# Kernel tuning notes

Measured on AMD Instinct MI355X. Metric: run time of the kernel, lower is better.

## Reference

```python
import jax, jax.numpy as jnp
import numpy as np

B, T, D, H = 2, 2048, 1024, 16
HD = D // H  # head_dim = 64


def setup_inputs() -> dict:
    key = jax.random.key(0)
    k1, k2, k3 = jax.random.split(key, 3)
    s = 0.02
    return {
        "x": jax.random.normal(k1, (B, T, D), dtype=jnp.float32),
        "Wqkv": jax.random.normal(k2, (D, 3 * D), dtype=jnp.float32) * s,
        "bqkv": jnp.zeros((3 * D,), dtype=jnp.float32),
        "Wout": jax.random.normal(k3, (D, D), dtype=jnp.float32) * s,
        "bout": jnp.zeros((D,), dtype=jnp.float32),
    }


def reference(x, Wqkv, bqkv, Wout, bout):
    Bx, Tx, Dx = x.shape
    qkv = x @ Wqkv + bqkv                                  # [B,T,3D]
    qkv = qkv.reshape(Bx, Tx, 3, H, HD)
    q, k, v = (jnp.moveaxis(qkv, 2, 0)[i] for i in range(3))  # each [B,T,H,HD]
    q = q.transpose(0, 2, 1, 3)  # [B,H,T,HD]
    k = k.transpose(0, 2, 1, 3)
    v = v.transpose(0, 2, 1, 3)
    scale = 1.0 / jnp.sqrt(jnp.float32(HD))
    attn = jnp.einsum("bhqd,bhkd->bhqk", q, k) * scale     # [B,H,T,T]
    causal = jnp.tril(jnp.ones((Tx, Tx), dtype=bool))
    attn = jnp.where(causal, attn, -jnp.inf)
    attn = jax.nn.softmax(attn, axis=-1)
    out = jnp.einsum("bhqk,bhkd->bhqd", attn, v)           # [B,H,T,HD]
    out = out.transpose(0, 2, 1, 3).reshape(Bx, Tx, Dx)
    return out @ Wout + bout
```

## Files before the change

### kernel.cpp

```cpp
#include <hip/hip_runtime.h>
#include <hip/hip_bf16.h>

typedef __attribute__((ext_vector_type(8))) short bf16x8;
typedef __attribute__((ext_vector_type(4))) float f32x4;
typedef unsigned short u16;
typedef unsigned int uint;

#define Bb 2
#define Tt 2048
#define Dd 1024
#define Hh 16

__device__ inline u16 f2bf(float f) {
    union { float f; uint u; } v; v.f = f;
    uint r = v.u + 0x7fffu + ((v.u >> 16) & 1u);
    return (u16)(r >> 16);
}

__global__ __launch_bounds__(256) void cvt_bf16(
    const float* __restrict__ in, u16* __restrict__ out)
{
    const size_t i = ((size_t)blockIdx.x * 256 + threadIdx.x) * 8;
    const float4 a = *(const float4*)&in[i];
    const float4 b = *(const float4*)&in[i + 4];
    uint4 o;
    o.x = (uint)f2bf(a.x) | ((uint)f2bf(a.y) << 16);
    o.y = (uint)f2bf(a.z) | ((uint)f2bf(a.w) << 16);
    o.z = (uint)f2bf(b.x) | ((uint)f2bf(b.y) << 16);
    o.w = (uint)f2bf(b.z) | ((uint)f2bf(b.w) << 16);
    *(uint4*)&out[i] = o;
}

__global__ __launch_bounds__(256) void transpose_cvt(
    const float* __restrict__ W, u16* __restrict__ Wt, int K, int N)
{
    __shared__ float tile[64][65];
    const int k0 = blockIdx.y * 64, n0 = blockIdx.x * 64;
    const int tid = threadIdx.x;
    const int tr = tid >> 4;
    const int tc = (tid & 15) * 4;

    #pragma unroll
    for (int i = 0; i < 4; ++i) {
        const float4 v = *(const float4*)&W[(size_t)(k0 + tr + i * 16) * N + n0 + tc];
        tile[tr + i * 16][tc + 0] = v.x;
        tile[tr + i * 16][tc + 1] = v.y;
        tile[tr + i * 16][tc + 2] = v.z;
        tile[tr + i * 16][tc + 3] = v.w;
    }
    __syncthreads();
    #pragma unroll
    for (int i = 0; i < 4; ++i) {
        ushort4 o;
        o.x = f2bf(tile[tc + 0][tr + i * 16]);
        o.y = f2bf(tile[tc + 1][tr + i * 16]);
        o.z = f2bf(tile[tc + 2][tr + i * 16]);
        o.w = f2bf(tile[tc + 3][tr + i * 16]);
        *(ushort4*)&Wt[(size_t)(n0 + tr + i * 16) * K + k0 + tc] = o;
    }
}

__global__ __launch_bounds__(256) void vtrans(
    const u16* __restrict__ qkvb, u16* __restrict__ vglob)
{
    __shared__ u16 ts[64 * 72];
    const int tt = blockIdx.x;
    const int hb = blockIdx.y;
    const int h = hb & 15, b = hb >> 4;
    const int tid = threadIdx.x;
    const int t0 = tt * 64;
    const size_t vbase = (size_t)((b * Hh + h) * 64) * Tt;

    #pragma unroll
    for (int j = 0; j < 2; ++j) {
        const int ci = tid + j * 256;
        const int t = ci >> 3, dc = ci & 7;
        *(int4*)&ts[t * 72 + dc * 8] =
            *(const int4*)&qkvb[(size_t)(b * Tt + t0 + t) * 3072 + 2048 + h * 64 + dc * 8];
    }
    __syncthreads();
    #pragma unroll
    for (int j = 0; j < 2; ++j) {
        const int ci = tid + j * 256;
        const int d = ci >> 3, tc = ci & 7;
        ushort4 lo, hi;
        lo.x = ts[(tc * 8 + 0) * 72 + d];
        lo.y = ts[(tc * 8 + 1) * 72 + d];
        lo.z = ts[(tc * 8 + 2) * 72 + d];
        lo.w = ts[(tc * 8 + 3) * 72 + d];
        hi.x = ts[(tc * 8 + 4) * 72 + d];
        hi.y = ts[(tc * 8 + 5) * 72 + d];
        hi.z = ts[(tc * 8 + 6) * 72 + d];
        hi.w = ts[(tc * 8 + 7) * 72 + d];
        *(ushort4*)&vglob[vbase + (size_t)d * Tt + t0 + tc * 8] = lo;
        *(ushort4*)&vglob[vbase + (size_t)d * Tt + t0 + tc * 8 + 4] = hi;
    }
}

template <int OUT_BF16>
__global__ __launch_bounds__(256) void gemm_bt(
    const u16* __restrict__ A, const u16* __restrict__ Bt,
    const float* __restrict__ bias, void* __restrict__ C,
    int M, int N, int K)
{
    __shared__ u16 As[128 * 40];
    __shared__ u16 Bs[128 * 40];

    const int tid  = threadIdx.x;
    const int lane = tid & 63;
    const int w    = tid >> 6;
    const int wm   = w >> 1, wn = w & 1;
    const int quad = lane >> 4;
    const int m16  = lane & 15;
    const int row0 = blockIdx.y * 128;
    const int col0 = blockIdx.x * 128;

    f32x4 acc[4][4];
    #pragma unroll
    for (int i = 0; i < 4; ++i)
        #pragma unroll
        for (int j = 0; j < 4; ++j) acc[i][j] = (f32x4){0.f, 0.f, 0.f, 0.f};

    const int r0s = tid >> 2,         k0s = tid & 3;
    const int r1s = (tid + 256) >> 2, k1s = tid & 3;

    for (int ko = 0; ko < K; ko += 32) {
        const int4 va0 = *(const int4*)&A [(size_t)(row0 + r0s) * K + ko + k0s * 8];
        const int4 va1 = *(const int4*)&A [(size_t)(row0 + r1s) * K + ko + k1s * 8];
        const int4 vb0 = *(const int4*)&Bt[(size_t)(col0 + r0s) * K + ko + k0s * 8];
        const int4 vb1 = *(const int4*)&Bt[(size_t)(col0 + r1s) * K + ko + k1s * 8];
        __syncthreads();
        *(int4*)&As[r0s * 40 + k0s * 8] = va0;
        *(int4*)&As[r1s * 40 + k1s * 8] = va1;
        *(int4*)&Bs[r0s * 40 + k0s * 8] = vb0;
        *(int4*)&Bs[r1s * 40 + k1s * 8] = vb1;
        __syncthreads();

        bf16x8 af[4], bfr[4];
        #pragma unroll
        for (int mt = 0; mt < 4; ++mt)
            af[mt] = *(const bf16x8*)&As[(wm * 64 + mt * 16 + m16) * 40 + quad * 8];
        #pragma unroll
        for (int nt = 0; nt < 4; ++nt)
            bfr[nt] = *(const bf16x8*)&Bs[(wn * 64 + nt * 16 + m16) * 40 + quad * 8];
        #pragma unroll
        for (int mt = 0; mt < 4; ++mt)
            #pragma unroll
            for (int nt = 0; nt < 4; ++nt)
                acc[mt][nt] = __builtin_amdgcn_mfma_f32_16x16x32_bf16(
                    af[mt], bfr[nt], acc[mt][nt], 0, 0, 0);
    }

    #pragma unroll
    for (int mt = 0; mt < 4; ++mt) {
        #pragma unroll
        for (int nt = 0; nt < 4; ++nt) {
            const int row = row0 + wm * 64 + mt * 16 + quad * 4;
            const int col = col0 + wn * 64 + nt * 16 + m16;
            const float bv = bias[col];
            #pragma unroll
            for (int r = 0; r < 4; ++r) {
                const float v = acc[mt][nt][r] + bv;
                if (OUT_BF16)
                    ((u16*)C)[(size_t)(row + r) * N + col] = f2bf(v);
                else
                    ((float*)C)[(size_t)(row + r) * N + col] = v;
            }
        }
    }
}

__global__ __launch_bounds__(256) void attn_mfma(
    const u16* __restrict__ qkvb, const u16* __restrict__ vglob,
    u16* __restrict__ attn_out)
{
    const int hb  = blockIdx.x;
    const int h   = hb & 15, b = hb >> 4;
    const int qt  = 15 - blockIdx.y;
    const int tid = threadIdx.x;
    const int lane = tid & 63, w = tid >> 6;
    const int quad = lane >> 4, m16 = lane & 15;

    __shared__ u16 S[20480];
    u16* Ks = S;
    u16* Vt = S + 4608;
    u16* Pt = S + 10240;
    u16* Ob = S;

    const int q0 = qt * 128;
    const size_t qkbase = (size_t)(b * Tt) * 3072;
    const size_t vbase  = (size_t)((b * Hh + h) * 64) * Tt;

    bf16x8 qb[2][2];
    #pragma unroll
    for (int nt = 0; nt < 2; ++nt)
        #pragma unroll
        for (int ks = 0; ks < 2; ++ks)
            qb[nt][ks] = *(const bf16x8*)&qkvb[
                qkbase + (size_t)(q0 + w * 32 + nt * 16 + m16) * 3072
                + h * 64 + ks * 32 + quad * 8];

    f32x4 o[4][2];
    #pragma unroll
    for (int ct = 0; ct < 4; ++ct)
        #pragma unroll
        for (int nt = 0; nt < 2; ++nt) o[ct][nt] = (f32x4){0.f, 0.f, 0.f, 0.f};
    float mst[2] = {-__builtin_inff(), -__builtin_inff()};
    float lst[2] = {0.f, 0.f};
    const float scale = 0.125f;

    const int ntiles = 2 * qt + 2;
    for (int kt = 0; kt < ntiles; ++kt) {
        const int k0 = kt * 64;
        __syncthreads();
        #pragma unroll
        for (int j = 0; j < 2; ++j) {
            const int ci = tid + j * 256;
            const int row = ci >> 3, kc = ci & 7;
            *(int4*)&Ks[row * 72 + kc * 8] = *(const int4*)&qkvb[
                qkbase + (size_t)(k0 + row) * 3072 + 1024 + h * 64 + kc * 8];
            *(int4*)&Vt[row * 72 + kc * 8] = *(const int4*)&vglob[
                vbase + (size_t)row * Tt + k0 + kc * 8];
        }
        __syncthreads();

        if (k0 <= q0 + w * 32 + 31) {
            bf16x8 ak[4][2];
            #pragma unroll
            for (int mt = 0; mt < 4; ++mt)
                #pragma unroll
                for (int ks = 0; ks < 2; ++ks)
                    ak[mt][ks] = *(const bf16x8*)&Ks[(mt * 16 + m16) * 72 + ks * 32 + quad * 8];
            f32x4 s[4][2];
            #pragma unroll
            for (int mt = 0; mt < 4; ++mt)
                #pragma unroll
                for (int nt = 0; nt < 2; ++nt) {
                    f32x4 a = (f32x4){0.f, 0.f, 0.f, 0.f};
                    a = __builtin_amdgcn_mfma_f32_16x16x32_bf16(ak[mt][0], qb[nt][0], a, 0, 0, 0);
                    a = __builtin_amdgcn_mfma_f32_16x16x32_bf16(ak[mt][1], qb[nt][1], a, 0, 0, 0);
                    s[mt][nt] = a;
                }

            const int qi0 = q0 + w * 32 + m16;
            if (k0 + 63 > q0 + w * 32) {
                #pragma unroll
                for (int mt = 0; mt < 4; ++mt)
                    #pragma unroll
                    for (int nt = 0; nt < 2; ++nt)
                        #pragma unroll
                        for (int r = 0; r < 4; ++r) {
                            const int key = k0 + mt * 16 + quad * 4 + r;
                            const float v = s[mt][nt][r] * scale;
                            s[mt][nt][r] = (key <= qi0 + nt * 16) ? v : -__builtin_inff();
                        }
            } else {
                #pragma unroll
                for (int mt = 0; mt < 4; ++mt)
                    #pragma unroll
                    for (int nt = 0; nt < 2; ++nt)
                        #pragma unroll
                        for (int r = 0; r < 4; ++r)
                            s[mt][nt][r] *= scale;
            }

            float mx[2] = {-__builtin_inff(), -__builtin_inff()};
            #pragma unroll
            for (int mt = 0; mt < 4; ++mt)
                #pragma unroll
                for (int nt = 0; nt < 2; ++nt)
                    #pragma unroll
                    for (int r = 0; r < 4; ++r)
                        mx[nt] = fmaxf(mx[nt], s[mt][nt][r]);
            #pragma unroll
            for (int nt = 0; nt < 2; ++nt) {
                mx[nt] = fmaxf(mx[nt], __shfl_xor(mx[nt], 16));
                mx[nt] = fmaxf(mx[nt], __shfl_xor(mx[nt], 32));
            }
            float al[2], ls[2];
            #pragma unroll
            for (int nt = 0; nt < 2; ++nt) {
                const float mn = fmaxf(mst[nt], mx[nt]);
                al[nt] = __expf(mst[nt] - mn);
                mst[nt] = mn;
                ls[nt] = 0.f;
            }
            #pragma unroll
            for (int mt = 0; mt < 4; ++mt)
                #pragma unroll
                for (int nt = 0; nt < 2; ++nt) {
                    ushort4 pk;
                    float p0 = __expf(s[mt][nt][0] - mst[nt]);
                    float p1 = __expf(s[mt][nt][1] - mst[nt]);
                    float p2 = __expf(s[mt][nt][2] - mst[nt]);
                    float p3 = __expf(s[mt][nt][3] - mst[nt]);
                    ls[nt] += (p0 + p1) + (p2 + p3);
                    pk.x = f2bf(p0); pk.y = f2bf(p1); pk.z = f2bf(p2); pk.w = f2bf(p3);
                    *(ushort4*)&Pt[(w * 32 + nt * 16 + m16) * 80 + mt * 16 + quad * 4] = pk;
                }
            #pragma unroll
            for (int nt = 0; nt < 2; ++nt) {
                ls[nt] += __shfl_xor(ls[nt], 16);
                ls[nt] += __shfl_xor(ls[nt], 32);
                lst[nt] = lst[nt] * al[nt] + ls[nt];
            }
            #pragma unroll
            for (int ct = 0; ct < 4; ++ct)
                #pragma unroll
                for (int nt = 0; nt < 2; ++nt)
                    #pragma unroll
                    for (int r = 0; r < 4; ++r)
                        o[ct][nt][r] *= al[nt];

            bf16x8 av[4][2], pb[2][2];
            #pragma unroll
            for (int ct = 0; ct < 4; ++ct)
                #pragma unroll
                for (int ks = 0; ks < 2; ++ks)
                    av[ct][ks] = *(const bf16x8*)&Vt[(ct * 16 + m16) * 72 + ks * 32 + quad * 8];
            #pragma unroll
            for (int nt = 0; nt < 2; ++nt)
                #pragma unroll
                for (int ks = 0; ks < 2; ++ks)
                    pb[nt][ks] = *(const bf16x8*)&Pt[(w * 32 + nt * 16 + m16) * 80 + ks * 32 + quad * 8];
            #pragma unroll
            for (int ct = 0; ct < 4; ++ct)
                #pragma unroll
                for (int nt = 0; nt < 2; ++nt) {
                    o[ct][nt] = __builtin_amdgcn_mfma_f32_16x16x32_bf16(av[ct][0], pb[nt][0], o[ct][nt], 0, 0, 0);
                    o[ct][nt] = __builtin_amdgcn_mfma_f32_16x16x32_bf16(av[ct][1], pb[nt][1], o[ct][nt], 0, 0, 0);
                }
        }
    }

    float invl[2];
    invl[0] = 1.0f / lst[0];
    invl[1] = 1.0f / lst[1];
    __syncthreads();
    #pragma unroll
    for (int ct = 0; ct < 4; ++ct)
        #pragma unroll
        for (int nt = 0; nt < 2; ++nt) {
            ushort4 pk;
            pk.x = f2bf(o[ct][nt][0] * invl[nt]);
            pk.y = f2bf(o[ct][nt][1] * invl[nt]);
            pk.z = f2bf(o[ct][nt][2] * invl[nt]);
            pk.w = f2bf(o[ct][nt][3] * invl[nt]);
            *(ushort4*)&Ob[(w * 32 + nt * 16 + m16) * 80 + ct * 16 + quad * 4] = pk;
        }
    __syncthreads();
    #pragma unroll
    for (int j = 0; j < 4; ++j) {
        const int ci = tid + j * 256;
        const int q = ci >> 3, kc = ci & 7;
        const int4 v = *(const int4*)&Ob[q * 80 + kc * 8];
        *(int4*)&attn_out[(size_t)(b * Tt + q0 + q) * 1024 + h * 64 + kc * 8] = v;
    }
}

extern "C" void kernel_launch(void* const* d_in, const int* in_sizes, int n_in,
                              void* d_out, int out_size, void* d_ws, size_t ws_size,
                              hipStream_t stream) {
    const float* x    = (const float*)d_in[0];
    const float* Wqkv = (const float*)d_in[1];
    const float* bqkv = (const float*)d_in[2];
    const float* Wout = (const float*)d_in[3];
    const float* bout = (const float*)d_in[4];
    float* out = (float*)d_out;

    u16* xb    = (u16*)d_ws;
    u16* WqT   = xb    + (size_t)4096 * 1024;
    u16* WoT   = WqT   + (size_t)3072 * 1024;
    u16* qkvb  = WoT   + (size_t)1024 * 1024;
    u16* attb  = qkvb  + (size_t)4096 * 3072;
    u16* vglob = attb  + (size_t)4096 * 1024;

    cvt_bf16<<<dim3((4096 * 1024) / 8 / 256), dim3(256), 0, stream>>>(x, xb);
    transpose_cvt<<<dim3(3072 / 64, 1024 / 64), dim3(256), 0, stream>>>(Wqkv, WqT, 1024, 3072);
    transpose_cvt<<<dim3(1024 / 64, 1024 / 64), dim3(256), 0, stream>>>(Wout, WoT, 1024, 1024);

    gemm_bt<1><<<dim3(3072 / 128, 4096 / 128), dim3(256), 0, stream>>>(
        xb, WqT, bqkv, qkvb, 4096, 3072, 1024);

    vtrans<<<dim3(Tt / 64, Hh * Bb), dim3(256), 0, stream>>>(qkvb, vglob);

    attn_mfma<<<dim3(Hh * Bb, Tt / 128), dim3(256), 0, stream>>>(qkvb, vglob, attb);

    gemm_bt<0><<<dim3(1024 / 128, 4096 / 128), dim3(256), 0, stream>>>(
        attb, WoT, bout, out, 4096, 1024, 1024);
}
```

Baseline: 219.4 us.

## Use direct global-to-LDS loads with XOR swizzle and double-buffer attention K/V

Both the GEMM and attention kernels now fill shared memory with global_load_lds, which writes 16-byte chunks straight into LDS instead of routing them through registers. An XOR-swizzled layout replaces the padded row stride to avoid LDS bank conflicts. The attention kernel also double-buffers K/V tiles, prefetching the next tile while the current one is computed, and drops one barrier per iteration. This relies on the compiler emitting the right waitcnt before the barrier for the async LDS loads. The double buffer raises the attention kernel's LDS footprint.

```diff
diff --git a/kernel.cpp b/kernel.cpp
--- a/kernel.cpp
+++ b/kernel.cpp
@@ -15,6 +15,13 @@
     union { float f; uint u; } v; v.f = f;
     uint r = v.u + 0x7fffu + ((v.u >> 16) & 1u);
     return (u16)(r >> 16);
+}
+
+__device__ inline void glds16(const u16* g, u16* l) {
+    __builtin_amdgcn_global_load_lds(
+        (const __attribute__((address_space(1))) void*)g,
+        (__attribute__((address_space(3))) void*)l,
+        16, 0, 0);
 }
 
 __global__ __launch_bounds__(256) void cvt_bf16(
@@ -103,8 +110,8 @@
     const float* __restrict__ bias, void* __restrict__ C,
     int M, int N, int K)
 {
-    __shared__ u16 As[128 * 40];
-    __shared__ u16 Bs[128 * 40];
+    __shared__ u16 As[128 * 32];
+    __shared__ u16 Bs[128 * 32];
 
     const int tid  = threadIdx.x;
     const int lane = tid & 63;
@@ -121,28 +128,26 @@
         #pragma unroll
         for (int j = 0; j < 4; ++j) acc[i][j] = (f32x4){0.f, 0.f, 0.f, 0.f};
 
-    const int r0s = tid >> 2,         k0s = tid & 3;
-    const int r1s = (tid + 256) >> 2, k1s = tid & 3;
+    const int sr  = tid >> 2, sqs = tid & 3;
+    const int sq  = sqs ^ ((sr >> 1) & 3);
+    const int ldsw = w * 512;
+    const int slot = quad ^ ((m16 >> 1) & 3);
 
     for (int ko = 0; ko < K; ko += 32) {
-        const int4 va0 = *(const int4*)&A [(size_t)(row0 + r0s) * K + ko + k0s * 8];
-        const int4 va1 = *(const int4*)&A [(size_t)(row0 + r1s) * K + ko + k1s * 8];
-        const int4 vb0 = *(const int4*)&Bt[(size_t)(col0 + r0s) * K + ko + k0s * 8];
-        const int4 vb1 = *(const int4*)&Bt[(size_t)(col0 + r1s) * K + ko + k1s * 8];
         __syncthreads();
-        *(int4*)&As[r0s * 40 + k0s * 8] = va0;
-        *(int4*)&As[r1s * 40 + k1s * 8] = va1;
-        *(int4*)&Bs[r0s * 40 + k0s * 8] = vb0;
-        *(int4*)&Bs[r1s * 40 + k1s * 8] = vb1;
+        glds16(&A [(size_t)(row0 + sr) * K + ko + sq * 8],       &As[ldsw]);
+        glds16(&A [(size_t)(row0 + sr + 64) * K + ko + sq * 8],  &As[2048 + ldsw]);
+        glds16(&Bt[(size_t)(col0 + sr) * K + ko + sq * 8],       &Bs[ldsw]);
+        glds16(&Bt[(size_t)(col0 + sr + 64) * K + ko + sq * 8],  &Bs[2048 + ldsw]);
         __syncthreads();
 
         bf16x8 af[4], bfr[4];
         #pragma unroll
         for (int mt = 0; mt < 4; ++mt)
-            af[mt] = *(const bf16x8*)&As[(wm * 64 + mt * 16 + m16) * 40 + quad * 8];
+            af[mt] = *(const bf16x8*)&As[(wm * 64 + mt * 16 + m16) * 32 + slot * 8];
         #pragma unroll
         for (int nt = 0; nt < 4; ++nt)
-            bfr[nt] = *(const bf16x8*)&Bs[(wn * 64 + nt * 16 + m16) * 40 + quad * 8];
+            bfr[nt] = *(const bf16x8*)&Bs[(wn * 64 + nt * 16 + m16) * 32 + slot * 8];
         #pragma unroll
         for (int mt = 0; mt < 4; ++mt)
             #pragma unroll
@@ -181,15 +186,17 @@
     const int lane = tid & 63, w = tid >> 6;
     const int quad = lane >> 4, m16 = lane & 15;
 
-    __shared__ u16 S[20480];
-    u16* Ks = S;
-    u16* Vt = S + 4608;
-    u16* Pt = S + 10240;
-    u16* Ob = S;
+    __shared__ u16 KV[2][2][64 * 64];
+    __shared__ u16 Pt[128 * 72];
 
     const int q0 = qt * 128;
     const size_t qkbase = (size_t)(b * Tt) * 3072;
     const size_t vbase  = (size_t)((b * Hh + h) * 64) * Tt;
+
+    const int sr8 = tid >> 3;
+    const int sq8 = (tid & 7) ^ (sr8 & 7);
+    const int ldsw = w * 512;
+    const int slot = quad ^ (m16 & 7);
 
     bf16x8 qb[2][2];
     #pragma unroll
@@ -200,6 +207,15 @@
                 qkbase + (size_t)(q0 + w * 32 + nt * 16 + m16) * 3072
                 + h * 64 + ks * 32 + quad * 8];
 
+    #pragma unroll
+    for (int j = 0; j < 2; ++j) {
+        const int row = j * 32 + sr8;
+        glds16(&qkvb[qkbase + (size_t)row * 3072 + 1024 + h * 64 + sq8 * 8],
+               &KV[0][0][j * 2048 + ldsw]);
+        glds16(&vglob[vbase + (size_t)row * Tt + sq8 * 8],
+               &KV[0][1][j * 2048 + ldsw]);
+    }
+
     f32x4 o[4][2];
     #pragma unroll
     for (int ct = 0; ct < 4; ++ct)
@@ -212,25 +228,32 @@
     const int ntiles = 2 * qt + 2;
     for (int kt = 0; kt < ntiles; ++kt) {
         const int k0 = kt * 64;
+        const int cb = kt & 1;
         __syncthreads();
-        #pragma unroll
-        for (int j = 0; j < 2; ++j) {
-            const int ci = tid + j * 256;
-            const int row = ci >> 3, kc = ci & 7;
-            *(int4*)&Ks[row * 72 + kc * 8] = *(const int4*)&qkvb[
-                qkbase + (size_t)(k0 + row) * 3072 + 1024 + h * 64 + kc * 8];
-            *(int4*)&Vt[row * 72 + kc * 8] = *(const int4*)&vglob[
-                vbase + (size_t)row * Tt + k0 + kc * 8];
+
+        if (kt + 1 < ntiles) {
+            const int k1 = k0 + 64, nb = cb ^ 1;
+            #pragma unroll
+            for (int j = 0; j < 2; ++j) {
+                const int row = j * 32 + sr8;
+                glds16(&qkvb[qkbase + (size_t)(k1 + row) * 3072 + 1024 + h * 64 + sq8 * 8],
+                       &KV[nb][0][j * 2048 + ldsw]);
+                glds16(&vglob[vbase + (size_t)row * Tt + k1 + sq8 * 8],
+                       &KV[nb][1][j * 2048 + ldsw]);
+            }
         }
-        __syncthreads();
 
         if (k0 <= q0 + w * 32 + 31) {
+            const u16* Ks = KV[cb][0];
+            const u16* Vt = KV[cb][1];
+
             bf16x8 ak[4][2];
             #pragma unroll
-            for (int mt = 0; mt < 4; ++mt)
-                #pragma unroll
-                for (int ks = 0; ks < 2; ++ks)
-                    ak[mt][ks] = *(const bf16x8*)&Ks[(mt * 16 + m16) * 72 + ks * 32 + quad * 8];
+            for (int mt = 0; mt < 4; ++mt) {
+                const int ro = (mt * 16 + m16) * 64;
+                ak[mt][0] = *(const bf16x8*)&Ks[ro + slot * 8];
+                ak[mt][1] = *(const bf16x8*)&Ks[ro + (slot ^ 4) * 8];
+            }
             f32x4 s[4][2];
             #pragma unroll
             for (int mt = 0; mt < 4; ++mt)
@@ -296,7 +319,7 @@
                     float p3 = __expf(s[mt][nt][3] - mst[nt]);
                     ls[nt] += (p0 + p1) + (p2 + p3);
                     pk.x = f2bf(p0); pk.y = f2bf(p1); pk.z = f2bf(p2); pk.w = f2bf(p3);
-                    *(ushort4*)&Pt[(w * 32 + nt * 16 + m16) * 80 + mt * 16 + quad * 4] = pk;
+                    *(ushort4*)&Pt[(w * 32 + nt * 16 + m16) * 72 + mt * 16 + quad * 4] = pk;
                 }
             #pragma unroll
             for (int nt = 0; nt < 2; ++nt) {
@@ -314,15 +337,16 @@
 
             bf16x8 av[4][2], pb[2][2];
             #pragma unroll
-            for (int ct = 0; ct < 4; ++ct)
+            for (int ct = 0; ct < 4; ++ct) {
+                const int ro = (ct * 16 + m16) * 64;
+                av[ct][0] = *(const bf16x8*)&Vt[ro + slot * 8];
+                av[ct][1] = *(const bf16x8*)&Vt[ro + (slot ^ 4) * 8];
+            }
+            #pragma unroll
+            for (int nt = 0; nt < 2; ++nt)
                 #pragma unroll
                 for (int ks = 0; ks < 2; ++ks)
-                    av[ct][ks] = *(const bf16x8*)&Vt[(ct * 16 + m16) * 72 + ks * 32 + quad * 8];
-            #pragma unroll
-            for (int nt = 0; nt < 2; ++nt)
-                #pragma unroll
-                for (int ks = 0; ks < 2; ++ks)
-                    pb[nt][ks] = *(const bf16x8*)&Pt[(w * 32 + nt * 16 + m16) * 80 + ks * 32 + quad * 8];
+                    pb[nt][ks] = *(const bf16x8*)&Pt[(w * 32 + nt * 16 + m16) * 72 + ks * 32 + quad * 8];
             #pragma unroll
             for (int ct = 0; ct < 4; ++ct)
                 #pragma unroll
@@ -336,7 +360,6 @@
     float invl[2];
     invl[0] = 1.0f / lst[0];
     invl[1] = 1.0f / lst[1];
-    __syncthreads();
     #pragma unroll
     for (int ct = 0; ct < 4; ++ct)
         #pragma unroll
@@ -346,14 +369,14 @@
             pk.y = f2bf(o[ct][nt][1] * invl[nt]);
             pk.z = f2bf(o[ct][nt][2] * invl[nt]);
             pk.w = f2bf(o[ct][nt][3] * invl[nt]);
-            *(ushort4*)&Ob[(w * 32 + nt * 16 + m16) * 80 + ct * 16 + quad * 4] = pk;
+            *(ushort4*)&Pt[(w * 32 + nt * 16 + m16) * 72 + ct * 16 + quad * 4] = pk;
         }
     __syncthreads();
     #pragma unroll
     for (int j = 0; j < 4; ++j) {
         const int ci = tid + j * 256;
         const int q = ci >> 3, kc = ci & 7;
-        const int4 v = *(const int4*)&Ob[q * 80 + kc * 8];
+        const int4 v = *(const int4*)&Pt[q * 72 + kc * 8];
         *(int4*)&attn_out[(size_t)(b * Tt + q0 + q) * 1024 + h * 64 + kc * 8] = v;
     }
 }
```

Result: no change. 218.7 us (-0.3%).
